# Optimization experiments

Hardware: AMD Instinct MI355X
Metric: run time of the kernel (lower is better)

## Reference

```python
import jax, jax.numpy as jnp
import numpy as np

N, IN, HID, OUT, E = 50000, 128, 128, 1, 800000
NEG_SLOPE = 0.2

def setup_inputs() -> dict:
    key = jax.random.key(0)
    ks = jax.random.split(key, 16)
    s = 0.05
    return {
        "x": jax.random.normal(ks[0], (N, IN), jnp.float32),
        "edge_index": jax.random.randint(ks[1], (2, E), 0, N, jnp.int64),
        "W1l": jax.random.normal(ks[2], (IN, HID), jnp.float32) * s,
        "b1l": jnp.zeros((HID,), jnp.float32),
        "W1r": jax.random.normal(ks[3], (IN, HID), jnp.float32) * s,
        "b1r": jnp.zeros((HID,), jnp.float32),
        "att1": jax.random.normal(ks[4], (HID,), jnp.float32) * s,
        "bias1": jnp.zeros((HID,), jnp.float32),
        "W2l": jax.random.normal(ks[5], (HID, OUT), jnp.float32) * s,
        "b2l": jnp.zeros((OUT,), jnp.float32),
        "W2r": jax.random.normal(ks[6], (HID, OUT), jnp.float32) * s,
        "b2r": jnp.zeros((OUT,), jnp.float32),
        "att2": jax.random.normal(ks[7], (OUT,), jnp.float32) * s,
        "bias2": jnp.zeros((OUT,), jnp.float32),
    }

def _gatv2(x, src, dst, Wl, bl, Wr, br, att, bias, n_nodes):
    # GATv2 single-head: e = att . LeakyReLU(Wl x_src + Wr x_dst)
    xl = x @ Wl + bl  # [N, H]
    xr = x @ Wr + br  # [N, H]
    e = jax.nn.leaky_relu(xl[src] + xr[dst], NEG_SLOPE) @ att  # [E]
    m = jax.ops.segment_max(e, dst, num_segments=n_nodes)       # per-dst max
    ex = jnp.exp(e - m[dst])
    denom = jax.ops.segment_sum(ex, dst, num_segments=n_nodes)
    alpha = ex / denom[dst]                                     # neighbor softmax
    out = jax.ops.segment_sum(xl[src] * alpha[:, None], dst, num_segments=n_nodes)
    return out + bias

def reference(x, edge_index, W1l, b1l, W1r, b1r, att1, bias1,
              W2l, b2l, W2r, b2r, att2, bias2):
    n = x.shape[0]
    loops = jnp.arange(n, dtype=edge_index.dtype)
    src = jnp.concatenate([edge_index[0], loops])  # add_self_loops=True
    dst = jnp.concatenate([edge_index[1], loops])
    h = _gatv2(x, src, dst, W1l, b1l, W1r, b1r, att1, bias1, n)
    h = jax.nn.relu(h)
    # dropout is identity at inference (training=False)
    h = _gatv2(h, src, dst, W2l, b2l, W2r, b2r, att2, bias2, n)
    out = jax.nn.sigmoid(h).squeeze()  # [N]
    return (out, out, out)
```

## Files before the change

### kernel.cpp

```cpp
#include <hip/hip_runtime.h>
#include <math.h>

#define NEG_SLOPE 0.2f
#define BCAP 6144

typedef __attribute__((ext_vector_type(8))) short short8;
typedef __attribute__((ext_vector_type(4))) float f32x4;

static __device__ __forceinline__ float lrelu(float t) { return t > 0.f ? t : NEG_SLOPE * t; }
static __device__ __forceinline__ float bf2f(unsigned short h) {
  union { unsigned int i; float f; } c; c.i = ((unsigned int)h) << 16; return c.f;
}
static __device__ __forceinline__ unsigned short f2bf(float x) {
  union { float f; unsigned int i; } c; c.f = x;
  unsigned int r = (c.i + 0x7fffu + ((c.i >> 16) & 1u)) >> 16;
  return (unsigned short)r;
}
static __device__ __forceinline__ void unpack8(uint4 u, float* f) {
  unsigned int d[4] = {u.x, u.y, u.z, u.w};
#pragma unroll
  for (int i = 0; i < 4; ++i) {
    union { unsigned int i_; float f_; } lo, hi;
    lo.i_ = d[i] << 16;
    hi.i_ = d[i] & 0xffff0000u;
    f[2 * i] = lo.f_;
    f[2 * i + 1] = hi.f_;
  }
}

__global__ __launch_bounds__(256) void k_bucket(const int* __restrict__ srcI, const int* __restrict__ dstI,
                                                int* __restrict__ gcur, uint2* __restrict__ pairs, int e) {
  __shared__ int hist[256];
  __shared__ int base[256];
  const int t = threadIdx.x;
  int chunk = (e + gridDim.x - 1) / gridDim.x;
  int lo = blockIdx.x * chunk;
  int hi = lo + chunk; if (hi > e) hi = e;
  hist[t] = 0;
  __syncthreads();
  for (int i = lo + t; i < hi; i += 256) atomicAdd(&hist[dstI[i] >> 8], 1);
  __syncthreads();
  int h = hist[t];
  base[t] = h ? atomicAdd(&gcur[t], h) : 0;
  hist[t] = 0;
  __syncthreads();
  for (int i = lo + t; i < hi; i += 256) {
    int d = dstI[i];
    int b = d >> 8;
    int r = atomicAdd(&hist[b], 1);
    pairs[(size_t)b * BCAP + base[b] + r] = make_uint2((unsigned)d, (unsigned)srcI[i]);
  }
}

__global__ __launch_bounds__(256) void k_sortb(const uint2* __restrict__ pairs, const int* __restrict__ gcur,
                                               int* __restrict__ offs, int* __restrict__ csr,
                                               int n, int e, int nbkt) {
  __shared__ int cnt[256];
  __shared__ int pre[256];
  __shared__ int bb[256];
  const int t = threadIdx.x;
  const int b = blockIdx.x;
  bb[t] = (t < nbkt) ? gcur[t] : 0;
  __syncthreads();
  for (int off = 1; off < 256; off <<= 1) {
    int u = (t >= off) ? bb[t - off] : 0;
    __syncthreads();
    bb[t] += u;
    __syncthreads();
  }
  const int mybase = (b == 0) ? 0 : bb[b - 1];
  const int mycnt = bb[b] - mybase;
  const uint2* bp = pairs + (size_t)b * BCAP;
  cnt[t] = 0;
  __syncthreads();
  for (int i = t; i < mycnt; i += 256) atomicAdd(&cnt[bp[i].x & 255], 1);
  __syncthreads();
  pre[t] = cnt[t];
  __syncthreads();
  for (int off = 1; off < 256; off <<= 1) {
    int u = (t >= off) ? pre[t - off] : 0;
    __syncthreads();
    pre[t] += u;
    __syncthreads();
  }
  int d = b * 256 + t;
  if (d < n) offs[d] = mybase + pre[t] - cnt[t];
  if (b == nbkt - 1 && t == 0) offs[n] = e;
  cnt[t] = pre[t] - cnt[t];
  __syncthreads();
  for (int i = t; i < mycnt; i += 256) {
    uint2 pr = bp[i];
    int r = atomicAdd(&cnt[pr.x & 255], 1);
    csr[mybase + r] = (int)pr.y;
  }
}

__global__ __launch_bounds__(256) void k_cvtW(const float* __restrict__ Wl, const float* __restrict__ Wr,
                                              unsigned short* __restrict__ Wth,
                                              unsigned short* __restrict__ Wtl,
                                              int* __restrict__ gcur) {
  int tid = blockIdx.x * 256 + threadIdx.x;
  if (tid < 256) gcur[tid] = 0;
  int wsel = tid >> 14;
  int rem = tid & 16383;
  int k = rem >> 7, c = rem & 127;
  float v = wsel ? Wr[k * 128 + c] : Wl[k * 128 + c];
  unsigned short h = f2bf(v);
  unsigned short lo = f2bf(v - bf2f(h));
  Wth[(c + 128 * wsel) * 128 + k] = h;
  Wtl[(c + 128 * wsel) * 128 + k] = lo;
}

__global__ __launch_bounds__(256) void k_mfma(const float* __restrict__ X,
                                              const unsigned short* __restrict__ Wth,
                                              const unsigned short* __restrict__ Wtl,
                                              const float* __restrict__ bl, const float* __restrict__ br,
                                              const float* __restrict__ att,
                                              unsigned short* __restrict__ xlr,
                                              float* __restrict__ dl, float* __restrict__ dr, int n) {
  __shared__ __align__(16) char lds[40960];
  char* wh = lds;
  char* wlo = lds + 16384;
  char* xh = lds + 32768;
  char* xo = lds + 36864;
  const int t = threadIdx.x;
  const int w = t >> 6, l = t & 63;
  const int lr = l & 15, lg = l >> 4;
  const int R0 = blockIdx.x * 64;

  f32x4 acc[4][4];
#pragma unroll
  for (int m = 0; m < 4; ++m)
#pragma unroll
    for (int nn = 0; nn < 4; ++nn) acc[m][nn] = (f32x4)(0.f);

  for (int k0 = 0; k0 < 128; k0 += 32) {
    if (k0) __syncthreads();
#pragma unroll
    for (int i = 0; i < 4; ++i) {
      int flat = t + i * 256;
      int col = flat >> 2, kc = flat & 3;
      int sw = (col & 3) ^ ((col >> 2) & 3);
      int off = col * 64 + ((kc ^ sw) << 4);
      *(uint4*)(wh + off) = *(const uint4*)(Wth + col * 128 + k0 + kc * 8);
      *(uint4*)(wlo + off) = *(const uint4*)(Wtl + col * 128 + k0 + kc * 8);
    }
    {
      int row = t >> 2, kc = t & 3;
      int r = R0 + row;
      float4 v0 = make_float4(0.f, 0.f, 0.f, 0.f), v1 = v0;
      if (r < n) {
        const float* p = X + (size_t)r * 128 + k0 + kc * 8;
        v0 = *(const float4*)p;
        v1 = *(const float4*)(p + 4);
      }
      float xs[8] = {v0.x, v0.y, v0.z, v0.w, v1.x, v1.y, v1.z, v1.w};
      unsigned int hi[4], lo[4];
#pragma unroll
      for (int i = 0; i < 4; ++i) {
        unsigned short h0 = f2bf(xs[2 * i]), h1 = f2bf(xs[2 * i + 1]);
        unsigned short l0 = f2bf(xs[2 * i] - bf2f(h0)), l1 = f2bf(xs[2 * i + 1] - bf2f(h1));
        hi[i] = (unsigned int)h0 | ((unsigned int)h1 << 16);
        lo[i] = (unsigned int)l0 | ((unsigned int)l1 << 16);
      }
      int sw = (row & 3) ^ ((row >> 2) & 3);
      int off = row * 64 + ((kc ^ sw) << 4);
      *(uint4*)(xh + off) = make_uint4(hi[0], hi[1], hi[2], hi[3]);
      *(uint4*)(xo + off) = make_uint4(lo[0], lo[1], lo[2], lo[3]);
    }
    __syncthreads();
    short8 axh[4], axl[4];
#pragma unroll
    for (int m = 0; m < 4; ++m) {
      int row = m * 16 + lr;
      int sw = (row & 3) ^ ((row >> 2) & 3);
      int off = row * 64 + ((lg ^ sw) << 4);
      axh[m] = *(const short8*)(xh + off);
      axl[m] = *(const short8*)(xo + off);
    }
#pragma unroll
    for (int nn = 0; nn < 4; ++nn) {
      int col = w * 64 + nn * 16 + lr;
      int sw = (col & 3) ^ ((col >> 2) & 3);
      int off = col * 64 + ((lg ^ sw) << 4);
      short8 bh = *(const short8*)(wh + off);
      short8 bo = *(const short8*)(wlo + off);
#pragma unroll
      for (int m = 0; m < 4; ++m) {
        acc[m][nn] = __builtin_amdgcn_mfma_f32_16x16x32_bf16(bh, axh[m], acc[m][nn], 0, 0, 0);
        acc[m][nn] = __builtin_amdgcn_mfma_f32_16x16x32_bf16(bh, axl[m], acc[m][nn], 0, 0, 0);
        acc[m][nn] = __builtin_amdgcn_mfma_f32_16x16x32_bf16(bo, axh[m], acc[m][nn], 0, 0, 0);
      }
    }
  }
  __syncthreads();
  float* sred = (float*)lds;
  float part[4];
#pragma unroll
  for (int m = 0; m < 4; ++m) {
    float pm = 0.f;
#pragma unroll
    for (int nn = 0; nn < 4; ++nn) {
      int colb = w * 64 + nn * 16 + lg * 4;
      const float* bp = (colb < 128) ? bl : br;
      float4 bv = *(const float4*)(bp + (colb & 127));
      float4 avv = *(const float4*)(att + (colb & 127));
      f32x4 o = acc[m][nn];
      float v0 = o[0] + bv.x, v1 = o[1] + bv.y, v2 = o[2] + bv.z, v3 = o[3] + bv.w;
      int row = R0 + m * 16 + lr;
      if (row < n) {
        uint2 pk;
        pk.x = (unsigned int)f2bf(v0) | ((unsigned int)f2bf(v1) << 16);
        pk.y = (unsigned int)f2bf(v2) | ((unsigned int)f2bf(v3) << 16);
        *(uint2*)(xlr + (size_t)row * 256 + colb) = pk;
      }
      pm += v0 * avv.x + v1 * avv.y + v2 * avv.z + v3 * avv.w;
    }
    pm += __shfl_xor(pm, 16, 64);
    pm += __shfl_xor(pm, 32, 64);
    part[m] = pm;
  }
  if (lg == 0) {
#pragma unroll
    for (int m = 0; m < 4; ++m) sred[w * 64 + m * 16 + lr] = part[m];
  }
  __syncthreads();
  if (t < 128) {
    int row = t & 63;
    int half = t >> 6;
    if (R0 + row < n) {
      float sum = sred[half * 128 + row] + sred[half * 128 + 64 + row];
      (half ? dr : dl)[R0 + row] = 0.6f * sum;
    }
  }
}

__global__ __launch_bounds__(256) void k_gat1(const unsigned short* __restrict__ xlr,
                                              const float* __restrict__ dl, const float* __restrict__ dr,
                                              const float* __restrict__ att, const float* __restrict__ bias,
                                              const float* __restrict__ W2l, const float* __restrict__ b2l,
                                              const float* __restrict__ W2r, const float* __restrict__ b2r,
                                              const int* __restrict__ offs, const int* __restrict__ csr,
                                              float* __restrict__ hl, float* __restrict__ hr, int n) {
  int wave = (blockIdx.x * 256 + threadIdx.x) >> 6;
  int lane = threadIdx.x & 63;
  if (wave >= n) return;
  const int v = wave;
  const int g = lane >> 4;
  const int q = lane & 15;
  const int cb = q * 8;

  float xrf[8];
  unpack8(*(const uint4*)(xlr + (size_t)v * 256 + 128 + cb), xrf);
  float av[8];
#pragma unroll
  for (int i = 0; i < 8; ++i) av[i] = att[cb + i];
  const float c0 = dr[v];

  float acc[8] = {0.f, 0.f, 0.f, 0.f, 0.f, 0.f, 0.f, 0.f};
  float denom = 0.f;
  const int s0 = offs[v], s1 = offs[v + 1];

  if (g == 0) {
    float dls = dl[v];
    float xf[8];
    unpack8(*(const uint4*)(xlr + (size_t)v * 256 + cb), xf);
    float s2 = 0.f;
#pragma unroll
    for (int i = 0; i < 8; ++i) s2 = fmaf(av[i], fabsf(xf[i] + xrf[i]), s2);
    s2 += __shfl_xor(s2, 1, 64);
    s2 += __shfl_xor(s2, 2, 64);
    s2 += __shfl_xor(s2, 4, 64);
    s2 += __shfl_xor(s2, 8, 64);
    float pe = __expf(fmaf(0.4f, s2, dls + c0));
    denom += pe;
#pragma unroll
    for (int i = 0; i < 8; ++i) acc[i] = fmaf(pe, xf[i], acc[i]);
  }

  for (int j = s0 + g; j < s1; j += 4) {
    int s = csr[j];
    float dls = dl[s];
    float xf[8];
    unpack8(*(const uint4*)(xlr + (size_t)s * 256 + cb), xf);
    float s2 = 0.f;
#pragma unroll
    for (int i = 0; i < 8; ++i) s2 = fmaf(av[i], fabsf(xf[i] + xrf[i]), s2);
    s2 += __shfl_xor(s2, 1, 64);
    s2 += __shfl_xor(s2, 2, 64);
    s2 += __shfl_xor(s2, 4, 64);
    s2 += __shfl_xor(s2, 8, 64);
    float pe = __expf(fmaf(0.4f, s2, dls + c0));
    denom += pe;
#pragma unroll
    for (int i = 0; i < 8; ++i) acc[i] = fmaf(pe, xf[i], acc[i]);
  }
#pragma unroll
  for (int off = 16; off <= 32; off <<= 1) {
#pragma unroll
    for (int i = 0; i < 8; ++i) acc[i] += __shfl_xor(acc[i], off, 64);
    denom += __shfl_xor(denom, off, 64);
  }
  float inv = 1.f / denom;
  float pl = 0.f, pr = 0.f;
#pragma unroll
  for (int i = 0; i < 8; ++i) {
    float h = fmaxf(acc[i] * inv + bias[cb + i], 0.f);
    pl += h * W2l[cb + i];
    pr += h * W2r[cb + i];
  }
#pragma unroll
  for (int off = 1; off <= 8; off <<= 1) {
    pl += __shfl_xor(pl, off, 64);
    pr += __shfl_xor(pr, off, 64);
  }
  if (lane == 0) {
    hl[v] = pl + b2l[0];
    hr[v] = pr + b2r[0];
  }
}

__global__ __launch_bounds__(256) void k_gat2(const float* __restrict__ hl, const float* __restrict__ hr,
                                              const float* __restrict__ att2, const float* __restrict__ bias2,
                                              const int* __restrict__ offs, const int* __restrict__ csr,
                                              float* __restrict__ out, int n) {
  int wave = (blockIdx.x * 256 + threadIdx.x) >> 6;
  int lane = threadIdx.x & 63;
  if (wave >= n) return;
  const int v = wave;
  const float a2 = att2[0];
  const float hrv = hr[v];
  float d = 0.f, num = 0.f;
  if (lane == 0) {
    float hlv = hl[v];
    float pe = __expf(a2 * lrelu(hlv + hrv));
    d += pe;
    num += pe * hlv;
  }
  const int s0 = offs[v], s1 = offs[v + 1];
  for (int j = s0 + lane; j < s1; j += 64) {
    int s = csr[j];
    float hls = hl[s];
    float pe = __expf(a2 * lrelu(hls + hrv));
    d += pe;
    num += pe * hls;
  }
#pragma unroll
  for (int off = 32; off; off >>= 1) {
    d += __shfl_xor(d, off, 64);
    num += __shfl_xor(num, off, 64);
  }
  if (lane == 0) {
    float z = num / d + bias2[0];
    float o = 1.f / (1.f + __expf(-z));
    out[v] = o;
    out[n + v] = o;
    out[2 * n + v] = o;
  }
}

extern "C" void kernel_launch(void* const* d_in, const int* in_sizes, int n_in,
                              void* d_out, int out_size, void* d_ws, size_t ws_size,
                              hipStream_t stream) {
  const float* x     = (const float*)d_in[0];
  const int*   ei    = (const int*)d_in[1];
  const float* W1l   = (const float*)d_in[2];
  const float* b1l   = (const float*)d_in[3];
  const float* W1r   = (const float*)d_in[4];
  const float* b1r   = (const float*)d_in[5];
  const float* att1  = (const float*)d_in[6];
  const float* bias1 = (const float*)d_in[7];
  const float* W2l   = (const float*)d_in[8];
  const float* b2l   = (const float*)d_in[9];
  const float* W2r   = (const float*)d_in[10];
  const float* b2r   = (const float*)d_in[11];
  const float* att2  = (const float*)d_in[12];
  const float* bias2 = (const float*)d_in[13];
  float* out = (float*)d_out;

  const int N = in_sizes[0] / 128;
  const int E = in_sizes[1] / 2;
  const int* srcI = ei;
  const int* dstI = ei + E;
  const int NBKT = (N + 255) >> 8;

  char* w = (char*)d_ws;
  auto alloc = [&](size_t bytes) {
    char* p = w;
    w += (bytes + 255) & ~(size_t)255;
    return p;
  };
  int* gcur  = (int*)alloc(1024);
  uint2* pairs = (uint2*)alloc((size_t)NBKT * BCAP * 8);
  int* offs  = (int*)alloc((size_t)(N + 1) * 4);
  int* csr   = (int*)alloc((size_t)E * 4);
  unsigned short* Wth = (unsigned short*)alloc(256 * 128 * 2);
  unsigned short* Wtl = (unsigned short*)alloc(256 * 128 * 2);
  unsigned short* xlr = (unsigned short*)alloc((size_t)N * 256 * 2);
  float* dl  = (float*)alloc((size_t)N * 4);
  float* dr  = (float*)alloc((size_t)N * 4);
  float* hl  = (float*)alloc((size_t)N * 4);
  float* hr  = (float*)alloc((size_t)N * 4);

  k_cvtW<<<128, 256, 0, stream>>>(W1l, W1r, Wth, Wtl, gcur);
  k_bucket<<<512, 256, 0, stream>>>(srcI, dstI, gcur, pairs, E);
  k_sortb<<<NBKT, 256, 0, stream>>>(pairs, gcur, offs, csr, N, E, NBKT);

  const int LB = (N + 63) / 64;
  k_mfma<<<LB, 256, 0, stream>>>(x, Wth, Wtl, b1l, b1r, att1, xlr, dl, dr, N);

  const int GB = (N + 3) / 4;
  k_gat1<<<GB, 256, 0, stream>>>(xlr, dl, dr, att1, bias1, W2l, b2l, W2r, b2r, offs, csr, hl, hr, N);
  k_gat2<<<GB, 256, 0, stream>>>(hl, hr, att2, bias2, offs, csr, out, N);
}
```

Baseline: 129.5 us.

## Merge preprocessing kernels into two launches running independent work side by side

Weight conversion and edge bucketing now share one launch, split by block index. Bucket sorting into CSR and the feature-transform MFMA GEMM now share another. This cuts the launch count from four to two (plus a memset that zeroes the counters) and lets independent work fill the GPU together instead of serializing small kernels. In exchange, the fused main kernel reserves the full 40 KB of LDS for its sort blocks too, which may limit occupancy.

```diff
diff --git a/kernel.cpp b/kernel.cpp
--- a/kernel.cpp
+++ b/kernel.cpp
@@ -28,105 +28,104 @@
   }
 }
 
-__global__ __launch_bounds__(256) void k_bucket(const int* __restrict__ srcI, const int* __restrict__ dstI,
-                                                int* __restrict__ gcur, uint2* __restrict__ pairs, int e) {
-  __shared__ int hist[256];
-  __shared__ int base[256];
+__global__ __launch_bounds__(256) void k_prep(const int* __restrict__ srcI, const int* __restrict__ dstI,
+                                              int* __restrict__ gcur, uint2* __restrict__ pairs, int e,
+                                              const float* __restrict__ Wl, const float* __restrict__ Wr,
+                                              unsigned short* __restrict__ Wth, unsigned short* __restrict__ Wtl) {
+  __shared__ int sh[512];
   const int t = threadIdx.x;
-  int chunk = (e + gridDim.x - 1) / gridDim.x;
-  int lo = blockIdx.x * chunk;
-  int hi = lo + chunk; if (hi > e) hi = e;
-  hist[t] = 0;
-  __syncthreads();
-  for (int i = lo + t; i < hi; i += 256) atomicAdd(&hist[dstI[i] >> 8], 1);
-  __syncthreads();
-  int h = hist[t];
-  base[t] = h ? atomicAdd(&gcur[t], h) : 0;
-  hist[t] = 0;
-  __syncthreads();
-  for (int i = lo + t; i < hi; i += 256) {
-    int d = dstI[i];
-    int b = d >> 8;
-    int r = atomicAdd(&hist[b], 1);
-    pairs[(size_t)b * BCAP + base[b] + r] = make_uint2((unsigned)d, (unsigned)srcI[i]);
-  }
-}
-
-__global__ __launch_bounds__(256) void k_sortb(const uint2* __restrict__ pairs, const int* __restrict__ gcur,
-                                               int* __restrict__ offs, int* __restrict__ csr,
-                                               int n, int e, int nbkt) {
-  __shared__ int cnt[256];
-  __shared__ int pre[256];
-  __shared__ int bb[256];
-  const int t = threadIdx.x;
-  const int b = blockIdx.x;
-  bb[t] = (t < nbkt) ? gcur[t] : 0;
-  __syncthreads();
-  for (int off = 1; off < 256; off <<= 1) {
-    int u = (t >= off) ? bb[t - off] : 0;
-    __syncthreads();
-    bb[t] += u;
-    __syncthreads();
-  }
-  const int mybase = (b == 0) ? 0 : bb[b - 1];
-  const int mycnt = bb[b] - mybase;
-  const uint2* bp = pairs + (size_t)b * BCAP;
-  cnt[t] = 0;
-  __syncthreads();
-  for (int i = t; i < mycnt; i += 256) atomicAdd(&cnt[bp[i].x & 255], 1);
-  __syncthreads();
-  pre[t] = cnt[t];
-  __syncthreads();
-  for (int off = 1; off < 256; off <<= 1) {
-    int u = (t >= off) ? pre[t - off] : 0;
-    __syncthreads();
-    pre[t] += u;
-    __syncthreads();
-  }
-  int d = b * 256 + t;
-  if (d < n) offs[d] = mybase + pre[t] - cnt[t];
-  if (b == nbkt - 1 && t == 0) offs[n] = e;
-  cnt[t] = pre[t] - cnt[t];
-  __syncthreads();
-  for (int i = t; i < mycnt; i += 256) {
-    uint2 pr = bp[i];
-    int r = atomicAdd(&cnt[pr.x & 255], 1);
-    csr[mybase + r] = (int)pr.y;
-  }
-}
-
-__global__ __launch_bounds__(256) void k_cvtW(const float* __restrict__ Wl, const float* __restrict__ Wr,
-                                              unsigned short* __restrict__ Wth,
-                                              unsigned short* __restrict__ Wtl,
-                                              int* __restrict__ gcur) {
-  int tid = blockIdx.x * 256 + threadIdx.x;
-  if (tid < 256) gcur[tid] = 0;
-  int wsel = tid >> 14;
-  int rem = tid & 16383;
-  int k = rem >> 7, c = rem & 127;
-  float v = wsel ? Wr[k * 128 + c] : Wl[k * 128 + c];
-  unsigned short h = f2bf(v);
-  unsigned short lo = f2bf(v - bf2f(h));
-  Wth[(c + 128 * wsel) * 128 + k] = h;
-  Wtl[(c + 128 * wsel) * 128 + k] = lo;
-}
-
-__global__ __launch_bounds__(256) void k_mfma(const float* __restrict__ X,
+  if (blockIdx.x < 512) {
+    int* hist = sh;
+    int* base = sh + 256;
+    int chunk = (e + 511) / 512;
+    int lo = blockIdx.x * chunk;
+    int hi = lo + chunk; if (hi > e) hi = e;
+    hist[t] = 0;
+    __syncthreads();
+    for (int i = lo + t; i < hi; i += 256) atomicAdd(&hist[dstI[i] >> 8], 1);
+    __syncthreads();
+    int h = hist[t];
+    base[t] = h ? atomicAdd(&gcur[t], h) : 0;
+    hist[t] = 0;
+    __syncthreads();
+    for (int i = lo + t; i < hi; i += 256) {
+      int d = dstI[i];
+      int b = d >> 8;
+      int r = atomicAdd(&hist[b], 1);
+      pairs[(size_t)b * BCAP + base[b] + r] = make_uint2((unsigned)d, (unsigned)srcI[i]);
+    }
+  } else {
+    int tid = (blockIdx.x - 512) * 256 + t;
+    int wsel = tid >> 14;
+    int rem = tid & 16383;
+    int k = rem >> 7, c = rem & 127;
+    float v = wsel ? Wr[k * 128 + c] : Wl[k * 128 + c];
+    unsigned short h = f2bf(v);
+    unsigned short lo = f2bf(v - bf2f(h));
+    Wth[(c + 128 * wsel) * 128 + k] = h;
+    Wtl[(c + 128 * wsel) * 128 + k] = lo;
+  }
+}
+
+__global__ __launch_bounds__(256) void k_main(const uint2* __restrict__ pairs, const int* __restrict__ gcur,
+                                              int* __restrict__ offs, int* __restrict__ csr,
+                                              int n, int e, int nbkt,
+                                              const float* __restrict__ X,
                                               const unsigned short* __restrict__ Wth,
                                               const unsigned short* __restrict__ Wtl,
                                               const float* __restrict__ bl, const float* __restrict__ br,
                                               const float* __restrict__ att,
                                               unsigned short* __restrict__ xlr,
-                                              float* __restrict__ dl, float* __restrict__ dr, int n) {
+                                              float* __restrict__ dl, float* __restrict__ dr) {
   __shared__ __align__(16) char lds[40960];
+  const int t = threadIdx.x;
+  if ((int)blockIdx.x < nbkt) {
+    int* cnt = (int*)lds;
+    int* pre = cnt + 256;
+    int* bb = pre + 256;
+    const int b = blockIdx.x;
+    bb[t] = (t < nbkt) ? gcur[t] : 0;
+    __syncthreads();
+    for (int off = 1; off < 256; off <<= 1) {
+      int u = (t >= off) ? bb[t - off] : 0;
+      __syncthreads();
+      bb[t] += u;
+      __syncthreads();
+    }
+    const int mybase = (b == 0) ? 0 : bb[b - 1];
+    const int mycnt = bb[b] - mybase;
+    const uint2* bp = pairs + (size_t)b * BCAP;
+    cnt[t] = 0;
+    __syncthreads();
+    for (int i = t; i < mycnt; i += 256) atomicAdd(&cnt[bp[i].x & 255], 1);
+    __syncthreads();
+    pre[t] = cnt[t];
+    __syncthreads();
+    for (int off = 1; off < 256; off <<= 1) {
+      int u = (t >= off) ? pre[t - off] : 0;
+      __syncthreads();
+      pre[t] += u;
+      __syncthreads();
+    }
+    int d = b * 256 + t;
+    if (d < n) offs[d] = mybase + pre[t] - cnt[t];
+    if (b == nbkt - 1 && t == 0) offs[n] = e;
+    cnt[t] = pre[t] - cnt[t];
+    __syncthreads();
+    for (int i = t; i < mycnt; i += 256) {
+      uint2 pr = bp[i];
+      int r = atomicAdd(&cnt[pr.x & 255], 1);
+      csr[mybase + r] = (int)pr.y;
+    }
+    return;
+  }
   char* wh = lds;
   char* wlo = lds + 16384;
   char* xh = lds + 32768;
   char* xo = lds + 36864;
-  const int t = threadIdx.x;
   const int w = t >> 6, l = t & 63;
   const int lr = l & 15, lg = l >> 4;
-  const int R0 = blockIdx.x * 64;
+  const int R0 = (blockIdx.x - nbkt) * 64;
 
   f32x4 acc[4][4];
 #pragma unroll
@@ -402,12 +401,12 @@
   float* hl  = (float*)alloc((size_t)N * 4);
   float* hr  = (float*)alloc((size_t)N * 4);
 
-  k_cvtW<<<128, 256, 0, stream>>>(W1l, W1r, Wth, Wtl, gcur);
-  k_bucket<<<512, 256, 0, stream>>>(srcI, dstI, gcur, pairs, E);
-  k_sortb<<<NBKT, 256, 0, stream>>>(pairs, gcur, offs, csr, N, E, NBKT);
-
   const int LB = (N + 63) / 64;
-  k_mfma<<<LB, 256, 0, stream>>>(x, Wth, Wtl, b1l, b1r, att1, xlr, dl, dr, N);
+
+  hipMemsetAsync(gcur, 0, 1024, stream);
+  k_prep<<<640, 256, 0, stream>>>(srcI, dstI, gcur, pairs, E, W1l, W1r, Wth, Wtl);
+  k_main<<<NBKT + LB, 256, 0, stream>>>(pairs, gcur, offs, csr, N, E, NBKT,
+                                        x, Wth, Wtl, b1l, b1r, att1, xlr, dl, dr);
 
   const int GB = (N + 3) / 4;
   k_gat1<<<GB, 256, 0, stream>>>(xlr, dl, dr, att1, bias1, W2l, b2l, W2r, b2r, offs, csr, hl, hr, N);
```

Result: faster. 117.7 us (-9.1%).
